# Optimization experiments

Hardware: AMD Instinct MI355X
Metric: run time of the kernel (lower is better)

The kernel has to match this reference:

```python
import jax, jax.numpy as jnp
import numpy as np

B, T, H = 64, 32, 768          # batch, num query tokens, hidden
E, NB, DFF = 8, 2, 3072        # num_experts, num_beams, expert ffn dim


def setup_inputs() -> dict:
    key = jax.random.key(0)
    ks = jax.random.split(key, 6)
    x = jax.random.normal(ks[0], (B, T, H), dtype=jnp.float32)
    gate_w = jax.random.normal(ks[1], (E, H), dtype=jnp.float32) * 0.02
    w1 = jax.random.normal(ks[2], (E, DFF, H), dtype=jnp.float32) * 0.02
    b1 = jnp.zeros((E, DFF), dtype=jnp.float32)
    w2 = jax.random.normal(ks[3], (E, H, DFF), dtype=jnp.float32) * 0.02
    b2 = jnp.zeros((E, H), dtype=jnp.float32)
    return {"x": x, "gate_w": gate_w, "w1": w1, "b1": b1, "w2": w2, "b2": b2}


def reference(x, gate_w, w1, b1, w2, b2):
    # ---- forward_gate: attention_mask is all ones -> plain mean over tokens ----
    x_avg = jnp.mean(x, axis=1)                         # [B, H]
    logits_gate = x_avg @ gate_w.T                      # [B, E]
    current_scores = jax.nn.softmax(logits_gate, axis=-1)

    # ---- importance auxiliary loss (torch.std is unbiased, ddof=1) ----
    importance = jnp.sum(current_scores, axis=0)        # [E]
    importance_loss = (jnp.std(importance, ddof=1) / jnp.mean(importance)) ** 2

    # ---- beam_search, first layer: exp(log(scores)) == scores; topk num_beams ----
    topk_vals, topk_idx = jax.lax.top_k(current_scores, NB)   # [B, NB]
    beam_scores = topk_vals.reshape(B * NB)
    expert_route = topk_idx.reshape(B * NB, 1).astype(jnp.int32)
    beam_idx = jnp.arange(B * NB, dtype=jnp.int32)

    # ---- replicate x / scores per beam: unsqueeze+expand+view == repeat ----
    x_rep = jnp.repeat(x, NB, axis=0)                   # [B*NB, T, H]
    scores_rep = jnp.repeat(current_scores, NB, axis=0) # [B*NB, E]
    input_x = x_rep[beam_idx]                           # identity gather (faithful)

    # ---- forward_expert_ffn: run ALL experts, then one-hot * prob combine ----
    h = jnp.einsum('bth,efh->betf', input_x, w1) + b1[None, :, None, :]
    h = jax.nn.gelu(h, approximate=False)               # torch nn.GELU default (exact)
    cand = jnp.einsum('betf,ehf->beth', h, w2) + b2[None, :, None, :]  # [B*NB, E, T, H]

    sel = expert_route[:, -1]                           # [B*NB]
    onehot = jax.nn.one_hot(sel, E, dtype=cand.dtype)   # [B*NB, E]
    weights = scores_rep * onehot                       # weight_type == 'ffn_prob'
    output = jnp.einsum('beth,be->bth', cand, weights)  # [B*NB, T, H]

    return output, beam_scores, expert_route, beam_idx, importance_loss
```

## Files before the change

kernel.cpp:

```cpp
#include <hip/hip_runtime.h>
#include <hip/hip_bf16.h>
#include <math.h>

#define Bsz 64
#define T 32
#define H 768
#define E 8
#define NB 2
#define DFF 3072
#define NBEAM (Bsz * NB)
#define NT4MAX 40

#define OUT_BS 3145728
#define OUT_ER 3145856
#define OUT_BI 3145984
#define OUT_IL 3146112

#define WS_LOGITS 0
#define WS_BEAMW  1536
#define WS_SORT   1664
#define WS_T4E    1792
#define WS_T4B    1832
#define WS_T4C    1872
#define WS_XBF    2048
#define WS_HBF    (2048 + 786432)

typedef __attribute__((ext_vector_type(8))) short short8;
typedef __attribute__((ext_vector_type(4))) float f32x4;

__device__ __forceinline__ short8 cvt8(const float4 u, const float4 v) {
    union { short8 s; unsigned w[4]; } r;
    __hip_bfloat162 t;
    t = __float22bfloat162_rn(make_float2(u.x, u.y)); r.w[0] = *(unsigned*)&t;
    t = __float22bfloat162_rn(make_float2(u.z, u.w)); r.w[1] = *(unsigned*)&t;
    t = __float22bfloat162_rn(make_float2(v.x, v.y)); r.w[2] = *(unsigned*)&t;
    t = __float22bfloat162_rn(make_float2(v.z, v.w)); r.w[3] = *(unsigned*)&t;
    return r.s;
}

__device__ __forceinline__ void async16(void* lds, const void* g) {
    __builtin_amdgcn_global_load_lds(
        (const __attribute__((address_space(1))) void*)g,
        (__attribute__((address_space(3))) void*)lds, 16, 0, 0);
}

__global__ __launch_bounds__(256) void conv_x_kernel(
    const float* __restrict__ x, ushort* __restrict__ xb, int n4)
{
    const int i = blockIdx.x * 256 + threadIdx.x;
    if (i >= n4) return;
    const float4 v = ((const float4*)x)[i];
    __hip_bfloat162 t0 = __float22bfloat162_rn(make_float2(v.x, v.y));
    __hip_bfloat162 t1 = __float22bfloat162_rn(make_float2(v.z, v.w));
    ushort4 o;
    o.x = (*(unsigned*)&t0) & 0xffff; o.y = (*(unsigned*)&t0) >> 16;
    o.z = (*(unsigned*)&t1) & 0xffff; o.w = (*(unsigned*)&t1) >> 16;
    ((ushort4*)xb)[i] = o;
}

__global__ __launch_bounds__(256) void gate_partial_kernel(
    const float* __restrict__ x, const float* __restrict__ gate_w,
    float* __restrict__ logits_part)
{
    __shared__ float part[4][E];
    const int chunk = blockIdx.x, b = blockIdx.y;
    const int tid = threadIdx.x, wv = tid >> 6, lane = tid & 63;
    const int c = chunk * 256 + tid;
    const float* xp = x + (size_t)b * T * H + c;
    float s = 0.f;
    #pragma unroll
    for (int t = 0; t < T; ++t) s += xp[t * H];
    const float avg = s * (1.0f / T);
    #pragma unroll
    for (int e = 0; e < E; ++e) {
        float p = avg * gate_w[e * H + c];
        #pragma unroll
        for (int off = 32; off; off >>= 1) p += __shfl_down(p, off, 64);
        if (lane == 0) part[wv][e] = p;
    }
    __syncthreads();
    if (tid < E) {
        float t = part[0][tid] + part[1][tid] + part[2][tid] + part[3][tid];
        logits_part[chunk * 512 + b * E + tid] = t;
    }
}

__global__ __launch_bounds__(64) void gating_kernel(
    const float* __restrict__ logits_part, float* __restrict__ beam_w,
    int* __restrict__ sortb, int* __restrict__ t4e, int* __restrict__ t4b,
    int* __restrict__ t4c, float* __restrict__ dout)
{
    const int r = threadIdx.x;
    float v[E];
    float mx = -1e30f;
    #pragma unroll
    for (int e = 0; e < E; ++e) {
        v[e] = logits_part[r * E + e] + logits_part[512 + r * E + e]
             + logits_part[1024 + r * E + e];
        mx = fmaxf(mx, v[e]);
    }
    float s = 0.f;
    #pragma unroll
    for (int e = 0; e < E; ++e) { v[e] = expf(v[e] - mx); s += v[e]; }
    const float inv = 1.0f / s;
    #pragma unroll
    for (int e = 0; e < E; ++e) v[e] *= inv;
    float v0 = -1.f, v1 = -1.f; int i0 = 0, i1 = 0;
    #pragma unroll
    for (int e = 0; e < E; ++e) {
        if (v[e] > v0)      { v1 = v0; i1 = i0; v0 = v[e]; i0 = e; }
        else if (v[e] > v1) { v1 = v[e]; i1 = e; }
    }
    const int b0 = 2 * r, b1 = 2 * r + 1;
    dout[OUT_BS + b0] = v0;          dout[OUT_BS + b1] = v1;
    dout[OUT_ER + b0] = (float)i0;   dout[OUT_ER + b1] = (float)i1;
    dout[OUT_BI + b0] = (float)b0;   dout[OUT_BI + b1] = (float)b1;
    beam_w[b0] = v0;  beam_w[b1] = v1;
    float imp[E];
    #pragma unroll
    for (int e = 0; e < E; ++e) {
        float t = v[e];
        #pragma unroll
        for (int off = 1; off < 64; off <<= 1) t += __shfl_xor(t, off, 64);
        imp[e] = t;
    }
    if (r == 0) {
        float tot = 0.f;
        #pragma unroll
        for (int e = 0; e < E; ++e) tot += imp[e];
        const float mean = tot / E;
        float var = 0.f;
        #pragma unroll
        for (int e = 0; e < E; ++e) { float d = imp[e] - mean; var += d * d; }
        var /= (E - 1);
        dout[OUT_IL] = var / (mean * mean);
    }
    unsigned long long m0[E], m1[E];
    #pragma unroll
    for (int e = 0; e < E; ++e) {
        m0[e] = __ballot(i0 == e);
        m1[e] = __ballot(i1 == e);
    }
    int cnt[E], off[E];
    int a0 = 0;
    #pragma unroll
    for (int e = 0; e < E; ++e) {
        cnt[e] = __popcll(m0[e]) + __popcll(m1[e]);
        off[e] = a0; a0 += cnt[e];
    }
    const unsigned long long below = (r == 0) ? 0ull : ((1ull << r) - 1ull);
    const unsigned long long incl  = below | (1ull << r);
    const int pos0 = __popcll(m0[i0] & below) + __popcll(m1[i0] & below);
    const int pos1 = __popcll(m0[i1] & incl)  + __popcll(m1[i1] & below);
    sortb[off[i0] + pos0] = b0;
    sortb[off[i1] + pos1] = b1;
    int tb[E]; int tc = 0;
    #pragma unroll
    for (int e = 0; e < E; ++e) { tb[e] = tc; tc += (cnt[e] + 3) >> 2; }
    if (r < E) {
        const int e = r;
        int j = tb[e];
        for (int i = 0; i < cnt[e]; i += 4, ++j) {
            t4e[j] = e;
            t4b[j] = off[e] + i;
            t4c[j] = (cnt[e] - i < 4) ? (cnt[e] - i) : 4;
        }
    }
    for (int t = tc + r; t < NT4MAX; t += 64) t4c[t] = 0;
}

template <int KTOT, int NTILE, bool DO_GELU>
__global__ __launch_bounds__(256, 2) void moe_ffn_mfma(
    const ushort* __restrict__ Abf, int a_div,
    const float* __restrict__ Wf32, int w_rows,
    const float* __restrict__ biasb,
    const int* __restrict__ sortb, const int* __restrict__ t4e,
    const int* __restrict__ t4b, const int* __restrict__ t4c,
    const float* __restrict__ beam_w,
    void* __restrict__ Obase)
{
    constexpr int KT = KTOT / 64;
    constexpr int WF = NTILE / 32;
    __shared__ __align__(16) ushort sA[2][128 * 64];
    __shared__ __align__(16) ushort sB[2][NTILE * 64];

    const int tile = blockIdx.y;
    const int cnt  = t4c[tile];
    if (cnt == 0) return;
    const int e    = t4e[tile];
    const int base = t4b[tile];
    const int tid  = threadIdx.x;
    const int wv   = tid >> 6;
    const int lane = tid & 63;
    const int quad = lane >> 4;
    const int l16  = lane & 15;
    const int mh   = (wv & 1) * 64;
    const int nh   = (wv >> 1) * (NTILE / 2);
    const int n0   = blockIdx.x * NTILE;

    int bm[4];
    #pragma unroll
    for (int s = 0; s < 4; ++s) bm[s] = sortb[base + (s < cnt ? s : cnt - 1)];

    const ushort* aseg[4];
    #pragma unroll
    for (int jj = 0; jj < 4; ++jj) {
        const int s = (wv * 4 + jj) * 64 + lane;
        const int r = s >> 3;
        const int c = (s & 7) ^ (r & 7);
        aseg[jj] = Abf + (size_t)(bm[r >> 5] / a_div) * T * KTOT
                 + (size_t)(r & 31) * KTOT + c * 8;
    }
    const float* wseg[WF];
    int wslot[WF];
    #pragma unroll
    for (int jj = 0; jj < WF; ++jj) {
        const int s = jj * 256 + tid;
        const int r = s >> 3;
        const int c = (s & 7) ^ (r & 7);
        wseg[jj] = Wf32 + (size_t)e * w_rows * KTOT + (size_t)(n0 + r) * KTOT + c * 8;
        wslot[jj] = s * 8;
    }

    int arow[4], ar7[4], brow[WF], br7[WF];
    #pragma unroll
    for (int mt = 0; mt < 4; ++mt) {
        const int r = mh + mt * 16 + l16;
        arow[mt] = r * 64; ar7[mt] = r & 7;
    }
    #pragma unroll
    for (int nt = 0; nt < WF; ++nt) {
        const int r = nh + nt * 16 + l16;
        brow[nt] = r * 64; br7[nt] = r & 7;
    }

    float4 wr[WF][2];
    #pragma unroll
    for (int jj = 0; jj < WF; ++jj) {
        wr[jj][0] = *(const float4*)(wseg[jj]);
        wr[jj][1] = *(const float4*)(wseg[jj] + 4);
    }
    #pragma unroll
    for (int jj = 0; jj < 4; ++jj)
        async16((char*)sA[0] + (wv * 4 + jj) * 1024, aseg[jj]);

    f32x4 acc[4][WF];
    #pragma unroll
    for (int mt = 0; mt < 4; ++mt)
        #pragma unroll
        for (int nt = 0; nt < WF; ++nt) acc[mt][nt] = {0.f, 0.f, 0.f, 0.f};

    for (int kt = 0; kt < KT; ++kt) {
        const int p = kt & 1;
        #pragma unroll
        for (int jj = 0; jj < WF; ++jj)
            *(short8*)(sB[p] + wslot[jj]) = cvt8(wr[jj][0], wr[jj][1]);
        __syncthreads();
        if (kt + 1 < KT) {
            const int kn = (kt + 1) * 64;
            #pragma unroll
            for (int jj = 0; jj < 4; ++jj)
                async16((char*)sA[1 - p] + (wv * 4 + jj) * 1024, aseg[jj] + kn);
            #pragma unroll
            for (int jj = 0; jj < WF; ++jj) {
                wr[jj][0] = *(const float4*)(wseg[jj] + kn);
                wr[jj][1] = *(const float4*)(wseg[jj] + kn + 4);
            }
        }
        #pragma unroll
        for (int ks = 0; ks < 2; ++ks) {
            short8 af[4], wf[WF];
            #pragma unroll
            for (int mt = 0; mt < 4; ++mt)
                af[mt] = *(const short8*)(sA[p] + arow[mt] + (((ks * 4 + quad) ^ ar7[mt]) * 8));
            #pragma unroll
            for (int nt = 0; nt < WF; ++nt)
                wf[nt] = *(const short8*)(sB[p] + brow[nt] + (((ks * 4 + quad) ^ br7[nt]) * 8));
            #pragma unroll
            for (int mt = 0; mt < 4; ++mt)
                #pragma unroll
                for (int nt = 0; nt < WF; ++nt)
                    acc[mt][nt] = __builtin_amdgcn_mfma_f32_16x16x32_bf16(
                        af[mt], wf[nt], acc[mt][nt], 0, 0, 0);
        }
    }

    #pragma unroll
    for (int nt = 0; nt < WF; ++nt) {
        const int n = n0 + nh + nt * 16 + l16;
        const float bias = biasb[(size_t)e * w_rows + n];
        #pragma unroll
        for (int mt = 0; mt < 4; ++mt) {
            const int rowb = mh + mt * 16 + quad * 4;
            const int s = rowb >> 5;
            if (s >= cnt) continue;
            const int b = bm[s];
            const float scale = DO_GELU ? 1.0f : beam_w[b];
            #pragma unroll
            for (int r = 0; r < 4; ++r) {
                const int t = (rowb + r) & 31;
                float vv = acc[mt][nt][r] + bias;
                const size_t idx = (size_t)b * T * w_rows + (size_t)t * w_rows + n;
                if (DO_GELU) {
                    vv = 0.5f * vv * (1.0f + erff(vv * 0.70710678118654752f));
                    ((__hip_bfloat16*)Obase)[idx] = __float2bfloat16(vv);
                } else {
                    ((float*)Obase)[idx] = vv * scale;
                }
            }
        }
    }
}

extern "C" void kernel_launch(void* const* d_in, const int* in_sizes, int n_in,
                              void* d_out, int out_size, void* d_ws, size_t ws_size,
                              hipStream_t stream)
{
    const float* x      = (const float*)d_in[0];
    const float* gate_w = (const float*)d_in[1];
    const float* w1     = (const float*)d_in[2];
    const float* b1     = (const float*)d_in[3];
    const float* w2     = (const float*)d_in[4];
    const float* b2     = (const float*)d_in[5];
    float* out = (float*)d_out;
    float* ws  = (float*)d_ws;

    float*  logits = ws + WS_LOGITS;
    float*  beam_w = ws + WS_BEAMW;
    int*    sortb  = (int*)(ws + WS_SORT);
    int*    t4e    = (int*)(ws + WS_T4E);
    int*    t4b    = (int*)(ws + WS_T4B);
    int*    t4c    = (int*)(ws + WS_T4C);
    ushort* x_bf   = (ushort*)(ws + WS_XBF);
    ushort* h_bf   = (ushort*)(ws + WS_HBF);

    conv_x_kernel<<<(Bsz * T * H / 4 + 255) / 256, 256, 0, stream>>>(
        x, x_bf, Bsz * T * H / 4);
    gate_partial_kernel<<<dim3(3, Bsz), 256, 0, stream>>>(x, gate_w, logits);
    gating_kernel<<<1, 64, 0, stream>>>(logits, beam_w, sortb, t4e, t4b, t4c, out);
    moe_ffn_mfma<H, 128, true><<<dim3(DFF / 128, NT4MAX), 256, 0, stream>>>(
        x_bf, NB, w1, DFF, b1, sortb, t4e, t4b, t4c, beam_w, (void*)h_bf);
    moe_ffn_mfma<DFF, 64, false><<<dim3(H / 64, NT4MAX), 256, 0, stream>>>(
        h_bf, 1, w2, H, b2, sortb, t4e, t4b, t4c, beam_w, out);
}
```

Before: 308.8 us.

## Use 256-row beam tiles with XCD-aware tile placement in MoE FFN GEMMs

Expert groups are now split into tiles of up to 8 beams (256 token rows) rather than 4. The GEMM kernel switches to a 256x64 block tile with K-step 32, so each fp32 weight tile is loaded and converted to bf16 once for twice as many rows. Block indices are remapped so each XCD mostly handles three fixed tile slots, with a single-thread scheduler filling overflow tiles into free slots. This cuts redundant weight traffic and conversion. In exchange it raises accumulator register pressure, halves the K depth per barrier, and may leave more padded rows unused for small experts.

```diff
diff --git a/kernel.cpp b/kernel.cpp
--- a/kernel.cpp
+++ b/kernel.cpp
@@ -9,7 +9,7 @@
 #define NB 2
 #define DFF 3072
 #define NBEAM (Bsz * NB)
-#define NT4MAX 40
+#define NT8MAX 24
 
 #define OUT_BS 3145728
 #define OUT_ER 3145856
@@ -19,9 +19,9 @@
 #define WS_LOGITS 0
 #define WS_BEAMW  1536
 #define WS_SORT   1664
-#define WS_T4E    1792
-#define WS_T4B    1832
-#define WS_T4C    1872
+#define WS_T8E    1792
+#define WS_T8B    1832
+#define WS_T8C    1872
 #define WS_XBF    2048
 #define WS_HBF    (2048 + 786432)
 
@@ -87,8 +87,8 @@
 
 __global__ __launch_bounds__(64) void gating_kernel(
     const float* __restrict__ logits_part, float* __restrict__ beam_w,
-    int* __restrict__ sortb, int* __restrict__ t4e, int* __restrict__ t4b,
-    int* __restrict__ t4c, float* __restrict__ dout)
+    int* __restrict__ sortb, int* __restrict__ t8e, int* __restrict__ t8b,
+    int* __restrict__ t8c, float* __restrict__ dout)
 {
     const int r = threadIdx.x;
     float v[E];
@@ -154,143 +154,150 @@
     const int pos1 = __popcll(m0[i1] & incl)  + __popcll(m1[i1] & below);
     sortb[off[i0] + pos0] = b0;
     sortb[off[i1] + pos1] = b1;
-    int tb[E]; int tc = 0;
-    #pragma unroll
-    for (int e = 0; e < E; ++e) { tb[e] = tc; tc += (cnt[e] + 3) >> 2; }
-    if (r < E) {
-        const int e = r;
-        int j = tb[e];
-        for (int i = 0; i < cnt[e]; i += 4, ++j) {
-            t4e[j] = e;
-            t4b[j] = off[e] + i;
-            t4c[j] = (cnt[e] - i < 4) ? (cnt[e] - i) : 4;
+    if (r == 0) {
+        int tiles[E];
+        int used[NT8MAX];
+        for (int t = 0; t < NT8MAX; ++t) used[t] = 0;
+        #pragma unroll
+        for (int e = 0; e < E; ++e) tiles[e] = (cnt[e] + 7) >> 3;
+        #pragma unroll
+        for (int e = 0; e < E; ++e) {
+            const int k = tiles[e] < 3 ? tiles[e] : 3;
+            for (int i = 0; i < k; ++i) {
+                const int sl = 3 * e + i;
+                t8e[sl] = e; t8b[sl] = off[e] + 8 * i;
+                const int rem = cnt[e] - 8 * i;
+                t8c[sl] = rem < 8 ? rem : 8;
+                used[sl] = 1;
+            }
         }
-    }
-    for (int t = tc + r; t < NT4MAX; t += 64) t4c[t] = 0;
-}
-
-template <int KTOT, int NTILE, bool DO_GELU>
+        int fs[NT8MAX]; int nf = 0;
+        for (int round = 0; round < 3; ++round)
+            for (int c = 0; c < E; ++c) {
+                const int sl = 3 * c + round;
+                if (!used[sl]) fs[nf++] = sl;
+            }
+        int fp = 0;
+        for (int e = 0; e < E; ++e)
+            for (int i = 3; i < tiles[e]; ++i) {
+                const int sl = fs[fp++];
+                t8e[sl] = e; t8b[sl] = off[e] + 8 * i;
+                const int rem = cnt[e] - 8 * i;
+                t8c[sl] = rem < 8 ? rem : 8;
+                used[sl] = 1;
+            }
+        for (int t = 0; t < NT8MAX; ++t) if (!used[t]) t8c[t] = 0;
+    }
+}
+
+template <int KTOT, bool DO_GELU>
 __global__ __launch_bounds__(256, 2) void moe_ffn_mfma(
     const ushort* __restrict__ Abf, int a_div,
     const float* __restrict__ Wf32, int w_rows,
     const float* __restrict__ biasb,
-    const int* __restrict__ sortb, const int* __restrict__ t4e,
-    const int* __restrict__ t4b, const int* __restrict__ t4c,
+    const int* __restrict__ sortb, const int* __restrict__ t8e,
+    const int* __restrict__ t8b, const int* __restrict__ t8c,
     const float* __restrict__ beam_w,
     void* __restrict__ Obase)
 {
-    constexpr int KT = KTOT / 64;
-    constexpr int WF = NTILE / 32;
-    __shared__ __align__(16) ushort sA[2][128 * 64];
-    __shared__ __align__(16) ushort sB[2][NTILE * 64];
-
-    const int tile = blockIdx.y;
-    const int cnt  = t4c[tile];
+    constexpr int KT = KTOT / 32;
+    __shared__ __align__(16) ushort sA[2][256 * 32];
+    __shared__ __align__(16) ushort sB[2][64 * 32];
+
+    const int nx  = gridDim.x;
+    const int hw  = blockIdx.y * nx + blockIdx.x;
+    const int xcd = hw & 7;
+    const int j   = hw >> 3;
+    const int tile  = 3 * xcd + j % 3;
+    const int strip = j / 3;
+
+    const int cnt  = t8c[tile];
     if (cnt == 0) return;
-    const int e    = t4e[tile];
-    const int base = t4b[tile];
+    const int e    = t8e[tile];
+    const int base = t8b[tile];
     const int tid  = threadIdx.x;
     const int wv   = tid >> 6;
     const int lane = tid & 63;
     const int quad = lane >> 4;
     const int l16  = lane & 15;
-    const int mh   = (wv & 1) * 64;
-    const int nh   = (wv >> 1) * (NTILE / 2);
-    const int n0   = blockIdx.x * NTILE;
-
-    int bm[4];
-    #pragma unroll
-    for (int s = 0; s < 4; ++s) bm[s] = sortb[base + (s < cnt ? s : cnt - 1)];
+    const int mh   = (wv & 1) * 128;
+    const int nh   = (wv >> 1) * 32;
+    const int n0   = strip * 64;
+
+    int bm[8];
+    #pragma unroll
+    for (int s = 0; s < 8; ++s) bm[s] = sortb[base + (s < cnt ? s : cnt - 1)];
 
     const ushort* aseg[4];
     #pragma unroll
     for (int jj = 0; jj < 4; ++jj) {
         const int s = (wv * 4 + jj) * 64 + lane;
-        const int r = s >> 3;
-        const int c = (s & 7) ^ (r & 7);
+        const int r = s >> 2;
+        const int c = (s & 3) ^ ((s >> 3) & 3);
         aseg[jj] = Abf + (size_t)(bm[r >> 5] / a_div) * T * KTOT
                  + (size_t)(r & 31) * KTOT + c * 8;
     }
-    const float* wseg[WF];
-    int wslot[WF];
-    #pragma unroll
-    for (int jj = 0; jj < WF; ++jj) {
-        const int s = jj * 256 + tid;
-        const int r = s >> 3;
-        const int c = (s & 7) ^ (r & 7);
-        wseg[jj] = Wf32 + (size_t)e * w_rows * KTOT + (size_t)(n0 + r) * KTOT + c * 8;
-        wslot[jj] = s * 8;
-    }
-
-    int arow[4], ar7[4], brow[WF], br7[WF];
-    #pragma unroll
-    for (int mt = 0; mt < 4; ++mt) {
-        const int r = mh + mt * 16 + l16;
-        arow[mt] = r * 64; ar7[mt] = r & 7;
-    }
-    #pragma unroll
-    for (int nt = 0; nt < WF; ++nt) {
-        const int r = nh + nt * 16 + l16;
-        brow[nt] = r * 64; br7[nt] = r & 7;
-    }
-
-    float4 wr[WF][2];
-    #pragma unroll
-    for (int jj = 0; jj < WF; ++jj) {
-        wr[jj][0] = *(const float4*)(wseg[jj]);
-        wr[jj][1] = *(const float4*)(wseg[jj] + 4);
-    }
+    const float* wseg;
+    int wslot;
+    {
+        const int r = tid >> 2;
+        const int c = (tid & 3) ^ ((tid >> 3) & 3);
+        wseg  = Wf32 + (size_t)e * w_rows * KTOT + (size_t)(n0 + r) * KTOT + c * 8;
+        wslot = tid * 8;
+    }
+
+    const int fx = (l16 >> 1) & 3;
+    int aoff[8], boff[2];
+    #pragma unroll
+    for (int mt = 0; mt < 8; ++mt)
+        aoff[mt] = (mh + mt * 16 + l16) * 32 + ((quad ^ fx) * 8);
+    #pragma unroll
+    for (int nt = 0; nt < 2; ++nt)
+        boff[nt] = (nh + nt * 16 + l16) * 32 + ((quad ^ fx) * 8);
+
+    float4 wr0 = *(const float4*)(wseg);
+    float4 wr1 = *(const float4*)(wseg + 4);
     #pragma unroll
     for (int jj = 0; jj < 4; ++jj)
         async16((char*)sA[0] + (wv * 4 + jj) * 1024, aseg[jj]);
 
-    f32x4 acc[4][WF];
-    #pragma unroll
-    for (int mt = 0; mt < 4; ++mt)
-        #pragma unroll
-        for (int nt = 0; nt < WF; ++nt) acc[mt][nt] = {0.f, 0.f, 0.f, 0.f};
+    f32x4 acc[8][2];
+    #pragma unroll
+    for (int mt = 0; mt < 8; ++mt) {
+        acc[mt][0] = {0.f, 0.f, 0.f, 0.f};
+        acc[mt][1] = {0.f, 0.f, 0.f, 0.f};
+    }
 
     for (int kt = 0; kt < KT; ++kt) {
         const int p = kt & 1;
-        #pragma unroll
-        for (int jj = 0; jj < WF; ++jj)
-            *(short8*)(sB[p] + wslot[jj]) = cvt8(wr[jj][0], wr[jj][1]);
+        *(short8*)(sB[p] + wslot) = cvt8(wr0, wr1);
         __syncthreads();
         if (kt + 1 < KT) {
-            const int kn = (kt + 1) * 64;
+            const int kn = (kt + 1) * 32;
             #pragma unroll
             for (int jj = 0; jj < 4; ++jj)
                 async16((char*)sA[1 - p] + (wv * 4 + jj) * 1024, aseg[jj] + kn);
-            #pragma unroll
-            for (int jj = 0; jj < WF; ++jj) {
-                wr[jj][0] = *(const float4*)(wseg[jj] + kn);
-                wr[jj][1] = *(const float4*)(wseg[jj] + kn + 4);
-            }
+            wr0 = *(const float4*)(wseg + kn);
+            wr1 = *(const float4*)(wseg + kn + 4);
         }
-        #pragma unroll
-        for (int ks = 0; ks < 2; ++ks) {
-            short8 af[4], wf[WF];
-            #pragma unroll
-            for (int mt = 0; mt < 4; ++mt)
-                af[mt] = *(const short8*)(sA[p] + arow[mt] + (((ks * 4 + quad) ^ ar7[mt]) * 8));
-            #pragma unroll
-            for (int nt = 0; nt < WF; ++nt)
-                wf[nt] = *(const short8*)(sB[p] + brow[nt] + (((ks * 4 + quad) ^ br7[nt]) * 8));
-            #pragma unroll
-            for (int mt = 0; mt < 4; ++mt)
-                #pragma unroll
-                for (int nt = 0; nt < WF; ++nt)
-                    acc[mt][nt] = __builtin_amdgcn_mfma_f32_16x16x32_bf16(
-                        af[mt], wf[nt], acc[mt][nt], 0, 0, 0);
+        const short8 wf0 = *(const short8*)(sB[p] + boff[0]);
+        const short8 wf1 = *(const short8*)(sB[p] + boff[1]);
+        #pragma unroll
+        for (int mt = 0; mt < 8; ++mt) {
+            const short8 af = *(const short8*)(sA[p] + aoff[mt]);
+            acc[mt][0] = __builtin_amdgcn_mfma_f32_16x16x32_bf16(
+                af, wf0, acc[mt][0], 0, 0, 0);
+            acc[mt][1] = __builtin_amdgcn_mfma_f32_16x16x32_bf16(
+                af, wf1, acc[mt][1], 0, 0, 0);
         }
     }
 
     #pragma unroll
-    for (int nt = 0; nt < WF; ++nt) {
+    for (int nt = 0; nt < 2; ++nt) {
         const int n = n0 + nh + nt * 16 + l16;
         const float bias = biasb[(size_t)e * w_rows + n];
         #pragma unroll
-        for (int mt = 0; mt < 4; ++mt) {
+        for (int mt = 0; mt < 8; ++mt) {
             const int rowb = mh + mt * 16 + quad * 4;
             const int s = rowb >> 5;
             if (s >= cnt) continue;
@@ -328,18 +335,18 @@
     float*  logits = ws + WS_LOGITS;
     float*  beam_w = ws + WS_BEAMW;
     int*    sortb  = (int*)(ws + WS_SORT);
-    int*    t4e    = (int*)(ws + WS_T4E);
-    int*    t4b    = (int*)(ws + WS_T4B);
-    int*    t4c    = (int*)(ws + WS_T4C);
+    int*    t8e    = (int*)(ws + WS_T8E);
+    int*    t8b    = (int*)(ws + WS_T8B);
+    int*    t8c    = (int*)(ws + WS_T8C);
     ushort* x_bf   = (ushort*)(ws + WS_XBF);
     ushort* h_bf   = (ushort*)(ws + WS_HBF);
 
     conv_x_kernel<<<(Bsz * T * H / 4 + 255) / 256, 256, 0, stream>>>(
         x, x_bf, Bsz * T * H / 4);
     gate_partial_kernel<<<dim3(3, Bsz), 256, 0, stream>>>(x, gate_w, logits);
-    gating_kernel<<<1, 64, 0, stream>>>(logits, beam_w, sortb, t4e, t4b, t4c, out);
-    moe_ffn_mfma<H, 128, true><<<dim3(DFF / 128, NT4MAX), 256, 0, stream>>>(
-        x_bf, NB, w1, DFF, b1, sortb, t4e, t4b, t4c, beam_w, (void*)h_bf);
-    moe_ffn_mfma<DFF, 64, false><<<dim3(H / 64, NT4MAX), 256, 0, stream>>>(
-        h_bf, 1, w2, H, b2, sortb, t4e, t4b, t4c, beam_w, out);
-}
+    gating_kernel<<<1, 64, 0, stream>>>(logits, beam_w, sortb, t8e, t8b, t8c, out);
+    moe_ffn_mfma<H, true><<<dim3(DFF / 64, NT8MAX), 256, 0, stream>>>(
+        x_bf, NB, w1, DFF, b1, sortb, t8e, t8b, t8c, beam_w, (void*)h_bf);
+    moe_ffn_mfma<DFF, false><<<dim3(H / 64, NT8MAX), 256, 0, stream>>>(
+        h_bf, 1, w2, H, b2, sortb, t8e, t8b, t8c, beam_w, out);
+}
```

Measured after the change: 375.2 us. +21.5%, slower.
